# Kernel tuning notes

Measured on AMD Instinct MI355X. Metric: run time of the kernel, lower is better.

The kernel has to match this reference:

```python
import jax, jax.numpy as jnp
import numpy as np

B, L, D = 16384, 6, 256
LN_EPS = 1e-5


def _layernorm(x, gamma, beta):
    mu = jnp.mean(x, axis=-1, keepdims=True)
    var = jnp.mean(jnp.square(x - mu), axis=-1, keepdims=True)
    return (x - mu) * jax.lax.rsqrt(var + LN_EPS) * gamma + beta


def _mlp_block(x, W, b, ln_g, ln_b):
    # Linear(D, D) -> LayerNorm(D) -> ReLU
    return jax.nn.relu(_layernorm(x @ W + b, ln_g, ln_b))


def setup_inputs() -> dict:
    key = jax.random.key(0)
    ks = jax.random.split(key, 8)
    s = 1.0 / np.sqrt(D)
    return {
        "gfeat": jax.random.normal(ks[0], (B, L, D), jnp.float32),
        "pfeat": jax.random.normal(ks[1], (B, L, D), jnp.float32),
        "Wg": jax.random.normal(ks[2], (D, D), jnp.float32) * s,
        "bg": jax.random.normal(ks[3], (D,), jnp.float32) * s,
        "g_ln_g": jnp.ones((D,), jnp.float32),
        "g_ln_b": jnp.zeros((D,), jnp.float32),
        "Wp": jax.random.normal(ks[4], (D, D), jnp.float32) * s,
        "bp": jax.random.normal(ks[5], (D,), jnp.float32) * s,
        "p_ln_g": jnp.ones((D,), jnp.float32),
        "p_ln_b": jnp.zeros((D,), jnp.float32),
        "wa_g": jax.random.normal(ks[6], (D,), jnp.float32) * s,
        "ba_g": jnp.zeros((), jnp.float32),
        "wa_p": jax.random.normal(ks[7], (D,), jnp.float32) * s,
        "ba_p": jnp.zeros((), jnp.float32),
    }


def reference(gfeat, pfeat, Wg, bg, g_ln_g, g_ln_b, Wp, bp, p_ln_g, p_ln_b,
              wa_g, ba_g, wa_p, ba_p):
    # g_align, p_align: [B, L, D]
    g_align = _mlp_block(gfeat, Wg, bg, g_ln_g, g_ln_b)
    p_align = _mlp_block(pfeat, Wp, bp, p_ln_g, p_ln_b)

    # Original torch code materializes atten[b,l,i,j] = g_align[b,l,i] * p_align[b,l,j]
    # ([B,L,D,D]) then applies Linear(D,1)+sigmoid along j (geno) / along i (path).
    # Mathematically:
    #   geno_att[b,l,i] = sigmoid(g_align[b,l,i] * (p_align[b,l] @ wa_g) + ba_g)
    #   path_att[b,l,j] = sigmoid(p_align[b,l,j] * (g_align[b,l] @ wa_p) + ba_p)
    # so we compute the bilinear reduction without forming the 4D tensor.
    p_red = jnp.einsum('bld,d->bl', p_align, wa_g)[..., None]  # [B,L,1]
    g_red = jnp.einsum('bld,d->bl', g_align, wa_p)[..., None]  # [B,L,1]
    geno_att = jax.nn.sigmoid(g_align * p_red + ba_g)
    path_att = jax.nn.sigmoid(p_align * g_red + ba_p)

    interaction = p_align * path_att + g_align * geno_att  # [B,L,D]
    return interaction
```

## Files before the change

kernel.cpp:

```cpp
#include <hip/hip_runtime.h>
#include <hip/hip_bf16.h>


typedef float f32x4 __attribute__((ext_vector_type(4)));
typedef short short8 __attribute__((ext_vector_type(8)));
typedef unsigned int u32;

#define D_DIM 256
#define ROWS 16
#define NW 4

union S8 { short8 s; u32 u[4]; };

__device__ __forceinline__ u32 f2bfu(float x) {
  u32 u = __float_as_uint(x);
  return (u + 0x7FFFu + ((u >> 16) & 1u)) >> 16;
}
__device__ __forceinline__ float sigm(float x) { return 1.0f / (1.0f + __expf(-x)); }

__device__ __forceinline__ u32 pk2c(float a, float b) {
  __hip_bfloat162 h = __float22bfloat162_rn(float2{a, b});
  union { __hip_bfloat162 h; u32 u; } cv;
  cv.h = h;
  return cv.u;
}

__global__ __launch_bounds__(256) void pack_w_kernel(const float* __restrict__ Wg,
                                                     const float* __restrict__ Wp,
                                                     unsigned short* __restrict__ outp) {
  int b = blockIdx.x;
  const float* W = (b < 32) ? Wg : Wp;
  unsigned short* o = outp + (b < 32 ? 0 : 65536);
  int chunk = (b & 31) * 256 + threadIdx.x;
  int c = chunk >> 9;
  int rest = chunk & 511;
  int t = rest >> 6;
  int l = rest & 63;
  int m = c * 16 + (l & 15);
  int kb = t * 32 + ((l >> 4) << 3);
  short8 v;
#pragma unroll
  for (int j = 0; j < 8; ++j) v[j] = (short)f2bfu(W[(kb + j) * 256 + m]);
  *(short8*)(o + (size_t)chunk * 8) = v;
}


__device__ __forceinline__ void stage_dma(const float* __restrict__ src, float* lbuf,
                                          int w, int lane) {
#pragma unroll
  for (int j = 0; j < 4; ++j) {
    int r = w * 4 + j;
    const float* gp = src + r * D_DIM + ((lane ^ (r & 7)) << 2);
    float* lp = lbuf + r * D_DIM;
    __builtin_amdgcn_global_load_lds(
        (const __attribute__((address_space(1))) u32*)gp,
        (__attribute__((address_space(3))) u32*)lp, 16, 0, 0);
  }
}

__device__ __forceinline__ void barrier_fence() {
  __builtin_amdgcn_s_barrier();
  asm volatile("" ::: "memory");
}

__device__ __forceinline__ short8 readAf32(const float* buf, int t, int lane) {
  const int cl = lane & 15, kg = lane >> 4;
  const int r = cl;
  const int s = r & 7;
  const int c16 = t * 8 + kg * 2;
  const char* base = (const char*)buf + r * 1024;
  float4 x = *(const float4*)(base + ((c16 ^ s) << 4));
  float4 y = *(const float4*)(base + (((c16 + 1) ^ s) << 4));
  S8 rr;
  rr.u[0] = pk2c(x.x, x.y);
  rr.u[1] = pk2c(x.z, x.w);
  rr.u[2] = pk2c(y.x, y.y);
  rr.u[3] = pk2c(y.z, y.w);
  return rr.s;
}

__device__ __forceinline__ void gemm4(f32x4 acc[4], const float* buf,
                                      const short8* __restrict__ wb, int lane, int w) {
  const int bbase = w * 2048 + lane;
#pragma unroll
  for (int h = 0; h < 2; ++h) {
    short8 a[4];
#pragma unroll
    for (int tt = 0; tt < 4; ++tt) a[tt] = readAf32(buf, h * 4 + tt, lane);
#pragma unroll
    for (int cp = 0; cp < 2; ++cp) {
      short8 bf[8];
#pragma unroll
      for (int c2 = 0; c2 < 2; ++c2)
#pragma unroll
        for (int tt = 0; tt < 4; ++tt)
          bf[c2 * 4 + tt] = wb[bbase + (cp * 2 + c2) * 512 + (h * 4 + tt) * 64];
#pragma unroll
      for (int c2 = 0; c2 < 2; ++c2)
#pragma unroll
        for (int tt = 0; tt < 4; ++tt)
          acc[cp * 2 + c2] =
              __builtin_amdgcn_mfma_f32_16x16x32_bf16(a[tt], bf[c2 * 4 + tt],
                                                      acc[cp * 2 + c2], 0, 0, 0);
    }
  }
}

__device__ __forceinline__ void statsPhase(f32x4 acc[4], const float bv[4],
                                           float smSum[NW][ROWS], float smSq[NW][ROWS],
                                           int lane, int w) {
#pragma unroll
  for (int r = 0; r < 4; ++r) {
    float s = 0.f, qq = 0.f;
#pragma unroll
    for (int c = 0; c < 4; ++c) {
      float y = acc[c][r] + bv[c];
      acc[c][r] = y;
      s += y; qq += y * y;
    }
#pragma unroll
    for (int m = 1; m < 16; m <<= 1) {
      s += __shfl_xor(s, m, 64);
      qq += __shfl_xor(qq, m, 64);
    }
    if ((lane & 15) == 0) {
      int row = ((lane >> 4) << 2) + r;
      smSum[w][row] = s;
      smSq[w][row] = qq;
    }
  }
}

__device__ __forceinline__ void applyPhase(f32x4 acc[4], f32x4 outAl[4],
                                           const float gv[4], const float tv[4], const float wv[4],
                                           const float smSum[NW][ROWS], const float smSq[NW][ROWS],
                                           float smRed[NW][ROWS], int lane, int w) {
#pragma unroll
  for (int r = 0; r < 4; ++r) {
    int row = ((lane >> 4) << 2) + r;
    float s = 0.f, qq = 0.f;
#pragma unroll
    for (int k = 0; k < NW; ++k) { s += smSum[k][row]; qq += smSq[k][row]; }
    float mu = s * (1.0f / 256.0f);
    float var = fmaxf(qq * (1.0f / 256.0f) - mu * mu, 0.0f);
    float rs = rsqrtf(var + 1e-5f);
    float dp = 0.f;
#pragma unroll
    for (int c = 0; c < 4; ++c) {
      float a = (acc[c][r] - mu) * rs * gv[c] + tv[c];
      a = fmaxf(a, 0.0f);
      outAl[c][r] = a;
      dp += a * wv[c];
    }
#pragma unroll
    for (int m = 1; m < 16; m <<= 1) dp += __shfl_xor(dp, m, 64);
    if ((lane & 15) == 0) smRed[w][row] = dp;
  }
}

__global__ __launch_bounds__(256, 4) void fused_main(
    const float* __restrict__ gfeat, const float* __restrict__ pfeat,
    const float* __restrict__ bg, const float* __restrict__ glng, const float* __restrict__ glnb,
    const float* __restrict__ bp, const float* __restrict__ plng, const float* __restrict__ plnb,
    const float* __restrict__ wag, const float* __restrict__ bag,
    const float* __restrict__ wap, const float* __restrict__ bap,
    const unsigned short* __restrict__ wpk,
    float* __restrict__ outp)
{
  __shared__ float bufA[ROWS * D_DIM];
  __shared__ float smSum[NW][ROWS], smSq[NW][ROWS], smRedG[NW][ROWS], smRedP[NW][ROWS];

  const int tid = threadIdx.x;
  const int lane = tid & 63;
  const int w = tid >> 6;
  const size_t row0 = (size_t)blockIdx.x * ROWS;

  const short8* wbg = (const short8*)wpk;
  const short8* wbp = (const short8*)(wpk + 65536);

  stage_dma(gfeat + row0 * D_DIM, bufA, w, lane);

  const int cb = w * 64 + (lane & 15);
  float bvG[4], bvP[4], gvG[4], tvG[4], wvG[4], gvP[4], tvP[4], wvP[4];
#pragma unroll
  for (int c = 0; c < 4; ++c) {
    bvG[c] = bg[cb + c * 16];
    bvP[c] = bp[cb + c * 16];
    gvG[c] = glng[cb + c * 16];
    tvG[c] = glnb[cb + c * 16];
    wvG[c] = wap[cb + c * 16];
    gvP[c] = plng[cb + c * 16];
    tvP[c] = plnb[cb + c * 16];
    wvP[c] = wag[cb + c * 16];
  }
  const float vbag = bag[0], vbap = bap[0];

  asm volatile("s_waitcnt vmcnt(0)" ::: "memory");
  barrier_fence();

  f32x4 accG[4];
#pragma unroll
  for (int c = 0; c < 4; ++c) accG[c] = {0.f, 0.f, 0.f, 0.f};
  gemm4(accG, bufA, wbg, lane, w);
  statsPhase(accG, bvG, smSum, smSq, lane, w);
  asm volatile("s_waitcnt lgkmcnt(0)" ::: "memory");
  barrier_fence();

  stage_dma(pfeat + row0 * D_DIM, bufA, w, lane);

  f32x4 alignG[4];
  applyPhase(accG, alignG, gvG, tvG, wvG, smSum, smSq, smRedG, lane, w);
  asm volatile("s_waitcnt vmcnt(0) lgkmcnt(0)" ::: "memory");
  barrier_fence();

  f32x4 accP[4];
#pragma unroll
  for (int c = 0; c < 4; ++c) accP[c] = {0.f, 0.f, 0.f, 0.f};
  gemm4(accP, bufA, wbp, lane, w);
  statsPhase(accP, bvP, smSum, smSq, lane, w);
  asm volatile("s_waitcnt lgkmcnt(0)" ::: "memory");
  barrier_fence();

  applyPhase(accP, accP, gvP, tvP, wvP, smSum, smSq, smRedP, lane, w);
  asm volatile("s_waitcnt lgkmcnt(0)" ::: "memory");
  barrier_fence();

#pragma unroll
  for (int r = 0; r < 4; ++r) {
    int row = ((lane >> 4) << 2) + r;
    float gr = 0.f, pr = 0.f;
#pragma unroll
    for (int k = 0; k < NW; ++k) { gr += smRedG[k][row]; pr += smRedP[k][row]; }
    float* orow = outp + (row0 + row) * D_DIM + w * 64 + (lane & 15);
#pragma unroll
    for (int c = 0; c < 4; ++c) {
      float ga = alignG[c][r];
      float pa = accP[c][r];
      float geno = sigm(ga * pr + vbag);
      float path = sigm(pa * gr + vbap);
      orow[c * 16] = pa * path + ga * geno;
    }
  }
}

extern "C" void kernel_launch(void* const* d_in, const int* in_sizes, int n_in,
                              void* d_out, int out_size, void* d_ws, size_t ws_size,
                              hipStream_t stream) {
  const float* gfeat = (const float*)d_in[0];
  const float* pfeat = (const float*)d_in[1];
  const float* Wg   = (const float*)d_in[2];
  const float* bg   = (const float*)d_in[3];
  const float* glng = (const float*)d_in[4];
  const float* glnb = (const float*)d_in[5];
  const float* Wp   = (const float*)d_in[6];
  const float* bp   = (const float*)d_in[7];
  const float* plng = (const float*)d_in[8];
  const float* plnb = (const float*)d_in[9];
  const float* wag  = (const float*)d_in[10];
  const float* bag  = (const float*)d_in[11];
  const float* wap  = (const float*)d_in[12];
  const float* bap  = (const float*)d_in[13];
  float* outp = (float*)d_out;
  unsigned short* wpk = (unsigned short*)d_ws;

  hipLaunchKernelGGL(pack_w_kernel, dim3(64), dim3(256), 0, stream, Wg, Wp, wpk);

  int nrows = in_sizes[0] / D_DIM;
  int nblocks = nrows / ROWS;
  hipLaunchKernelGGL(fused_main, dim3(nblocks), dim3(256), 0, stream,
                     gfeat, pfeat, bg, glng, glnb, bp, plng, plnb,
                     wag, bag, wap, bap, wpk, outp);
}
```

Measured before the change: 133.0 us.

## Stage both inputs up front into separate LDS buffers and merge phases

The kernel now DMAs the gfeat and pfeat tiles into two separate shared-memory buffers at the start, runs both GEMMs back-to-back, then does both LayerNorm stats and apply phases together. This removes two barriers and the serialized second load that previously waited on the first GEMM. LDS use doubles from 16KB to 32KB per block, which may lower occupancy under launch_bounds(256,4). The weight-fragment loop is also restructured to load 4 B fragments per output column instead of 8 at a time, which lowers register pressure.

```diff
diff --git a/kernel.cpp b/kernel.cpp
--- a/kernel.cpp
+++ b/kernel.cpp
@@ -88,26 +88,19 @@
 #pragma unroll
     for (int tt = 0; tt < 4; ++tt) a[tt] = readAf32(buf, h * 4 + tt, lane);
 #pragma unroll
-    for (int cp = 0; cp < 2; ++cp) {
-      short8 bf[8];
-#pragma unroll
-      for (int c2 = 0; c2 < 2; ++c2)
-#pragma unroll
-        for (int tt = 0; tt < 4; ++tt)
-          bf[c2 * 4 + tt] = wb[bbase + (cp * 2 + c2) * 512 + (h * 4 + tt) * 64];
-#pragma unroll
-      for (int c2 = 0; c2 < 2; ++c2)
-#pragma unroll
-        for (int tt = 0; tt < 4; ++tt)
-          acc[cp * 2 + c2] =
-              __builtin_amdgcn_mfma_f32_16x16x32_bf16(a[tt], bf[c2 * 4 + tt],
-                                                      acc[cp * 2 + c2], 0, 0, 0);
+    for (int c = 0; c < 4; ++c) {
+      short8 bf[4];
+#pragma unroll
+      for (int tt = 0; tt < 4; ++tt) bf[tt] = wb[bbase + c * 512 + (h * 4 + tt) * 64];
+#pragma unroll
+      for (int tt = 0; tt < 4; ++tt)
+        acc[c] = __builtin_amdgcn_mfma_f32_16x16x32_bf16(a[tt], bf[tt], acc[c], 0, 0, 0);
     }
   }
 }
 
 __device__ __forceinline__ void statsPhase(f32x4 acc[4], const float bv[4],
-                                           float smSum[NW][ROWS], float smSq[NW][ROWS],
+                                           float smS[NW][ROWS], float smQ[NW][ROWS],
                                            int lane, int w) {
 #pragma unroll
   for (int r = 0; r < 4; ++r) {
@@ -125,22 +118,22 @@
     }
     if ((lane & 15) == 0) {
       int row = ((lane >> 4) << 2) + r;
-      smSum[w][row] = s;
-      smSq[w][row] = qq;
+      smS[w][row] = s;
+      smQ[w][row] = qq;
     }
   }
 }
 
 __device__ __forceinline__ void applyPhase(f32x4 acc[4], f32x4 outAl[4],
                                            const float gv[4], const float tv[4], const float wv[4],
-                                           const float smSum[NW][ROWS], const float smSq[NW][ROWS],
+                                           const float smS[NW][ROWS], const float smQ[NW][ROWS],
                                            float smRed[NW][ROWS], int lane, int w) {
 #pragma unroll
   for (int r = 0; r < 4; ++r) {
     int row = ((lane >> 4) << 2) + r;
     float s = 0.f, qq = 0.f;
 #pragma unroll
-    for (int k = 0; k < NW; ++k) { s += smSum[k][row]; qq += smSq[k][row]; }
+    for (int k = 0; k < NW; ++k) { s += smS[k][row]; qq += smQ[k][row]; }
     float mu = s * (1.0f / 256.0f);
     float var = fmaxf(qq * (1.0f / 256.0f) - mu * mu, 0.0f);
     float rs = rsqrtf(var + 1e-5f);
@@ -167,8 +160,11 @@
     const unsigned short* __restrict__ wpk,
     float* __restrict__ outp)
 {
-  __shared__ float bufA[ROWS * D_DIM];
-  __shared__ float smSum[NW][ROWS], smSq[NW][ROWS], smRedG[NW][ROWS], smRedP[NW][ROWS];
+  __shared__ float bufG[ROWS * D_DIM];
+  __shared__ float bufP[ROWS * D_DIM];
+  __shared__ float smSG[NW][ROWS], smQG[NW][ROWS];
+  __shared__ float smSP[NW][ROWS], smQP[NW][ROWS];
+  __shared__ float smRG[NW][ROWS], smRP[NW][ROWS];
 
   const int tid = threadIdx.x;
   const int lane = tid & 63;
@@ -178,14 +174,33 @@
   const short8* wbg = (const short8*)wpk;
   const short8* wbp = (const short8*)(wpk + 65536);
 
-  stage_dma(gfeat + row0 * D_DIM, bufA, w, lane);
+  stage_dma(gfeat + row0 * D_DIM, bufG, w, lane);
+  stage_dma(pfeat + row0 * D_DIM, bufP, w, lane);
 
   const int cb = w * 64 + (lane & 15);
-  float bvG[4], bvP[4], gvG[4], tvG[4], wvG[4], gvP[4], tvP[4], wvP[4];
+  float bvG[4], bvP[4];
 #pragma unroll
   for (int c = 0; c < 4; ++c) {
     bvG[c] = bg[cb + c * 16];
     bvP[c] = bp[cb + c * 16];
+  }
+  const float vbag = bag[0], vbap = bap[0];
+
+  asm volatile("s_waitcnt vmcnt(0)" ::: "memory");
+  barrier_fence();
+
+  f32x4 accG[4], accP[4];
+#pragma unroll
+  for (int c = 0; c < 4; ++c) {
+    accG[c] = {0.f, 0.f, 0.f, 0.f};
+    accP[c] = {0.f, 0.f, 0.f, 0.f};
+  }
+  gemm4(accG, bufG, wbg, lane, w);
+  gemm4(accP, bufP, wbp, lane, w);
+
+  float gvG[4], tvG[4], wvG[4], gvP[4], tvP[4], wvP[4];
+#pragma unroll
+  for (int c = 0; c < 4; ++c) {
     gvG[c] = glng[cb + c * 16];
     tvG[c] = glnb[cb + c * 16];
     wvG[c] = wap[cb + c * 16];
@@ -193,35 +208,15 @@
     tvP[c] = plnb[cb + c * 16];
     wvP[c] = wag[cb + c * 16];
   }
-  const float vbag = bag[0], vbap = bap[0];
-
-  asm volatile("s_waitcnt vmcnt(0)" ::: "memory");
-  barrier_fence();
-
-  f32x4 accG[4];
-#pragma unroll
-  for (int c = 0; c < 4; ++c) accG[c] = {0.f, 0.f, 0.f, 0.f};
-  gemm4(accG, bufA, wbg, lane, w);
-  statsPhase(accG, bvG, smSum, smSq, lane, w);
+
+  statsPhase(accG, bvG, smSG, smQG, lane, w);
+  statsPhase(accP, bvP, smSP, smQP, lane, w);
   asm volatile("s_waitcnt lgkmcnt(0)" ::: "memory");
   barrier_fence();
 
-  stage_dma(pfeat + row0 * D_DIM, bufA, w, lane);
-
   f32x4 alignG[4];
-  applyPhase(accG, alignG, gvG, tvG, wvG, smSum, smSq, smRedG, lane, w);
-  asm volatile("s_waitcnt vmcnt(0) lgkmcnt(0)" ::: "memory");
-  barrier_fence();
-
-  f32x4 accP[4];
-#pragma unroll
-  for (int c = 0; c < 4; ++c) accP[c] = {0.f, 0.f, 0.f, 0.f};
-  gemm4(accP, bufA, wbp, lane, w);
-  statsPhase(accP, bvP, smSum, smSq, lane, w);
-  asm volatile("s_waitcnt lgkmcnt(0)" ::: "memory");
-  barrier_fence();
-
-  applyPhase(accP, accP, gvP, tvP, wvP, smSum, smSq, smRedP, lane, w);
+  applyPhase(accG, alignG, gvG, tvG, wvG, smSG, smQG, smRG, lane, w);
+  applyPhase(accP, accP,   gvP, tvP, wvP, smSP, smQP, smRP, lane, w);
   asm volatile("s_waitcnt lgkmcnt(0)" ::: "memory");
   barrier_fence();
 
@@ -230,7 +225,7 @@
     int row = ((lane >> 4) << 2) + r;
     float gr = 0.f, pr = 0.f;
 #pragma unroll
-    for (int k = 0; k < NW; ++k) { gr += smRedG[k][row]; pr += smRedP[k][row]; }
+    for (int k = 0; k < NW; ++k) { gr += smRG[k][row]; pr += smRP[k][row]; }
     float* orow = outp + (row0 + row) * D_DIM + w * 64 + (lane & 15);
 #pragma unroll
     for (int c = 0; c < 4; ++c) {
```

Measured after the change: 136.0 us. +2.2%, slower.
